# Kernel optimization log

Hardware: AMD Instinct MI355X
Metric: run time of the kernel (lower is better)

Reference implementation:

```python
import jax, jax.numpy as jnp
import numpy as np

NUM_NODES = 6144
INPUT_DIM = 128
OUTPUT_DIM = 128
NUM_HEADS = 4
HEAD_DIM = OUTPUT_DIM // NUM_HEADS
NEG_INF = -9e15  # mask constant used by the original module


def setup_inputs() -> dict:
    key = jax.random.key(0)
    k_x, k_adj, k_W, k_a = jax.random.split(key, 4)
    x = jax.random.normal(k_x, (NUM_NODES, INPUT_DIM), dtype=jnp.float32)
    adj = jax.random.randint(k_adj, (NUM_NODES, NUM_NODES), 0, 2, dtype=jnp.int32)
    # kaiming-uniform-ish init scale
    W = jax.random.uniform(k_W, (NUM_HEADS, INPUT_DIM, HEAD_DIM), dtype=jnp.float32,
                           minval=-1.0, maxval=1.0) * np.sqrt(6.0 / INPUT_DIM)
    a = jax.random.uniform(k_a, (NUM_HEADS, 2 * HEAD_DIM, 1), dtype=jnp.float32,
                           minval=-1.0, maxval=1.0) * np.sqrt(6.0 / (2 * HEAD_DIM))
    return {"x": x, "adj": adj, "W": W, "a": a}


def reference(x, adj, W, a):
    # x: [N, Din], adj: [N, N] int, W: [H, Din, d], a: [H, 2d, 1]
    H, Din, d = W.shape
    N = x.shape[0]
    h = jnp.einsum('ni,hid->hnd', x, W)               # [H, N, d] per-head projections
    a_dst = a[:, :d, 0]                                # applied to h_j (column / source of message)
    a_src = a[:, d:, 0]                                # applied to h_i (row / destination)
    s_dst = jnp.einsum('hnd,hd->hn', h, a_dst)         # [H, N]
    s_src = jnp.einsum('hnd,hd->hn', h, a_src)         # [H, N]
    # energy[h, i, j] = leaky_relu(a1 . h_j + a2 . h_i), same as concat-attention
    energy = jax.nn.leaky_relu(s_src[:, :, None] + s_dst[:, None, :], negative_slope=0.2)
    energy = jnp.where(adj[None] > 0, energy, NEG_INF)  # [H, N, N]
    attention = jax.nn.softmax(energy, axis=-1)
    h_prime = jnp.einsum('hij,hjd->hid', attention, h)  # [H, N, d]
    # faithful to torch h_prime.view(num_nodes, -1) on a contiguous [H,N,d] tensor
    return jnp.reshape(h_prime, (N, H * d))
```

## Files before the change

kernel.cpp:

```cpp
#include <hip/hip_runtime.h>
#include <stdint.h>

#define N_NODES 6144
#define LOG2E 1.44269504088896f

typedef float f32x4 __attribute__((ext_vector_type(4)));
typedef float f32x2 __attribute__((ext_vector_type(2)));
typedef short short8 __attribute__((ext_vector_type(8)));
typedef unsigned int uint32;
typedef unsigned long long uint64;

extern "C" __device__ float __ocml_native_exp2_f32(float);

__device__ __forceinline__ uint32 bitmask32(uint32 bits, int j) {
#if __has_builtin(__builtin_amdgcn_sbfe)
  return (uint32)__builtin_amdgcn_sbfe((int)bits, (uint32)j, 1u);
#else
  return (uint32)(((int)(bits << (31 - j))) >> 31);
#endif
}

__global__ __launch_bounds__(256) void k1_feat(const float* __restrict__ x,
                                               const float* __restrict__ W,
                                               const float* __restrict__ a,
                                               unsigned short* __restrict__ hfF,
                                               float* __restrict__ s_src2,
                                               float* __restrict__ s_dst2) {
  __shared__ float xA[8][132];
  __shared__ unsigned short tbp[128][12];
  int t = threadIdx.x;
  int bx = blockIdx.x;
  int n0 = bx << 3;
  {
    int row = t >> 5, c4 = (t & 31) << 2;
    *(float4*)&xA[row][c4] = *(const float4*)(x + (size_t)(n0 + row) * 128 + c4);
  }
  __syncthreads();
  int r = t & 7, cgA = t >> 3;
  int hh = cgA >> 3, d0 = (cgA & 7) << 2;
  const float* wp = W + hh * 4096 + d0;
  float ac0 = 0.f, ac1 = 0.f, ac2 = 0.f, ac3 = 0.f;
  #pragma unroll 8
  for (int i = 0; i < 128; ++i) {
    float xv = xA[r][i];
    float4 wv = *(const float4*)(wp + (i << 5));
    ac0 += xv * wv.x; ac1 += xv * wv.y;
    ac2 += xv * wv.z; ac3 += xv * wv.w;
  }
  int c0 = cgA << 2;
  tbp[c0 + 0][r] = (unsigned short)((__float_as_uint(ac0) + 0x8000u) >> 16);
  tbp[c0 + 1][r] = (unsigned short)((__float_as_uint(ac1) + 0x8000u) >> 16);
  tbp[c0 + 2][r] = (unsigned short)((__float_as_uint(ac2) + 0x8000u) >> 16);
  tbp[c0 + 3][r] = (unsigned short)((__float_as_uint(ac3) + 0x8000u) >> 16);
  float4 adv = *(const float4*)(a + hh * 64 + d0);
  float4 asv = *(const float4*)(a + hh * 64 + 32 + d0);
  float pd = ac0 * adv.x + ac1 * adv.y + ac2 * adv.z + ac3 * adv.w;
  float ps = ac0 * asv.x + ac1 * asv.y + ac2 * asv.z + ac3 * asv.w;
  pd += __shfl_xor(pd, 8); pd += __shfl_xor(pd, 16); pd += __shfl_xor(pd, 32);
  ps += __shfl_xor(ps, 8); ps += __shfl_xor(ps, 16); ps += __shfl_xor(ps, 32);
  if (((t & 63) >> 3) == 0) {
    s_dst2[hh * N_NODES + n0 + r] = pd * LOG2E;
    s_src2[hh * N_NODES + n0 + r] = ps * LOG2E;
  }
  __syncthreads();
  if (t < 128) {
    int h2 = t >> 5, ff = (t >> 4) & 1, mm = t & 15;
    const uint32* s32 = (const uint32*)&tbp[t][0];
    int4 v;
    v.x = s32[0]; v.y = s32[1]; v.z = s32[2]; v.w = s32[3];
    int kb = bx >> 2, qq = bx & 3;
    *(int4*)(hfF + (size_t)(((h2 * 192 + kb) * 2 + ff) * 64 + qq * 16 + mm) * 8) = v;
  }
}

__device__ __forceinline__ void gat_tile(float ss, uint32 bits8,
                                         const f32x2 (&dv)[4], short8 b0, short8 b1,
                                         short8 ones, f32x4& a0, f32x4& a1, f32x4& az) {
  union { uint32 u4[4]; short8 v; } afr;
  f32x2 ss2;
  ss2[0] = ss; ss2[1] = ss;
  #pragma unroll
  for (int p = 0; p < 4; ++p) {
    f32x2 e = ss2 + dv[p];
    f32x2 e5 = e * 0.2f;
    float lrl = fmaxf(e[0], e5[0]);
    float lrh = fmaxf(e[1], e5[1]);
    float exl = __ocml_native_exp2_f32(lrl);
    float exh = __ocml_native_exp2_f32(lrh);
    uint32 wl = __float_as_uint(exl) & bitmask32(bits8, 2 * p);
    uint32 wh = __float_as_uint(exh) & bitmask32(bits8, 2 * p + 1);
    uint32 pk;
    asm("v_cvt_pk_bf16_f32 %0, %1, %2"
        : "=v"(pk)
        : "v"(__uint_as_float(wl)), "v"(__uint_as_float(wh)));
    afr.u4[p] = pk;
  }
  a0 = __builtin_amdgcn_mfma_f32_16x16x32_bf16(afr.v, b0, a0, 0, 0, 0);
  a1 = __builtin_amdgcn_mfma_f32_16x16x32_bf16(afr.v, b1, a1, 0, 0, 0);
  az = __builtin_amdgcn_mfma_f32_16x16x32_bf16(afr.v, ones, az, 0, 0, 0);
}

__device__ __forceinline__ void step2(uint32 w0, uint32 w1,
                                      int sh, const float* sdp, int koff,
                                      int4 B0i, int4 B1i, short8 ones,
                                      float ss0, float ss1,
                                      f32x4& a00, f32x4& a01, f32x4& a10, f32x4& a11,
                                      f32x4& az0, f32x4& az1) {
  union { f32x4 q[2]; f32x2 d[4]; } du;
  du.q[0] = *(const f32x4*)(sdp + koff);
  du.q[1] = *(const f32x4*)(sdp + koff + 4);
  union { int4 i; short8 v; } b0u, b1u;
  b0u.i = B0i; b1u.i = B1i;
  gat_tile(ss0, (w0 >> sh), du.d, b0u.v, b1u.v, ones, a00, a01, az0);
  gat_tile(ss1, (w1 >> sh), du.d, b0u.v, b1u.v, ones, a10, a11, az1);
}

__global__ __launch_bounds__(256, 3) void k2_attn(const int* __restrict__ adj,
                                                  const unsigned short* __restrict__ hfF,
                                                  const float* __restrict__ s_src2,
                                                  const float* __restrict__ s_dst2,
                                                  float* __restrict__ Zpart,
                                                  float* __restrict__ part) {
  __shared__ float sd[4][1536];
  __shared__ uint32 mlds[2][32][4];
  int t = threadIdx.x;
  int h = t >> 6, lane = t & 63, m = lane & 15, quad = lane >> 4;
  int sh = quad << 3;
  int bx = blockIdx.x;
  int slice = bx & 3, mg = bx >> 2;
  int i0 = mg << 5, kbase = slice * 1536;

  const int* arow = adj + (size_t)(i0 + (h << 3)) * N_NODES + kbase + lane;
  int av[16];
  #pragma unroll
  for (int r = 0; r < 16; ++r)
    av[r] = arow[(r >> 1) * N_NODES + ((r & 1) << 6)];

  {
    const float4* g = (const float4*)s_dst2;
    float4* l = (float4*)sd;
    int kb4 = slice * 384;
    #pragma unroll
    for (int r = 0; r < 6; ++r) {
      int u = t + (r << 8);
      int hx = u / 384, uu = u - hx * 384;
      l[hx * 384 + uu] = g[hx * 1536 + kb4 + uu];
    }
  }
  float ss0 = s_src2[h * N_NODES + i0 + m];
  float ss1 = s_src2[h * N_NODES + i0 + 16 + m];
  #pragma unroll
  for (int r = 0; r < 16; ++r) {
    uint64 b = __ballot(av[r] != 0);
    if (lane == r)
      *(uint64*)&mlds[0][(h << 3) + (r >> 1)][(r & 1) << 1] = b;
  }
  __syncthreads();

  const unsigned short* hfb = hfF + (size_t)(h * 192 + slice * 48) * 1024 + lane * 8;
  const float* sdp = &sd[h][0] + sh;

  f32x4 a00 = {0,0,0,0}, a01 = {0,0,0,0};
  f32x4 a10 = {0,0,0,0}, a11 = {0,0,0,0};
  f32x4 az0 = {0,0,0,0}, az1 = {0,0,0,0};
  union { uint32 u[4]; short8 v; } ones;
  #pragma unroll
  for (int q = 0; q < 4; ++q) ones.u[q] = 0x3F803F80u;

  #pragma unroll 1
  for (int o = 0; o < 12; ++o) {
    int cur = o & 1, nxt = cur ^ 1;
    const unsigned short* gb = hfb + o * 4096;
    int4 B00 = *(const int4*)(gb);
    int4 B01 = *(const int4*)(gb + 512);
    int4 B10 = *(const int4*)(gb + 1024);
    int4 B11 = *(const int4*)(gb + 1536);
    int4 B20 = *(const int4*)(gb + 2048);
    int4 B21 = *(const int4*)(gb + 2560);
    int4 B30 = *(const int4*)(gb + 3072);
    int4 B31 = *(const int4*)(gb + 3584);
    int pv[16];
    if (o < 11) {
      const int* ap = arow + ((o + 1) << 7);
      #pragma unroll
      for (int r = 0; r < 16; ++r)
        pv[r] = ap[(r >> 1) * N_NODES + ((r & 1) << 6)];
    }
    uint4 M0 = *(const uint4*)&mlds[cur][m][0];
    uint4 M1 = *(const uint4*)&mlds[cur][16 + m][0];
    __builtin_amdgcn_sched_barrier(0);
    int ko = o << 7;
    step2(M0.x, M1.x, sh, sdp, ko,      B00, B01, ones.v, ss0, ss1,
          a00, a01, a10, a11, az0, az1);
    step2(M0.y, M1.y, sh, sdp, ko + 32, B10, B11, ones.v, ss0, ss1,
          a00, a01, a10, a11, az0, az1);
    step2(M0.z, M1.z, sh, sdp, ko + 64, B20, B21, ones.v, ss0, ss1,
          a00, a01, a10, a11, az0, az1);
    step2(M0.w, M1.w, sh, sdp, ko + 96, B30, B31, ones.v, ss0, ss1,
          a00, a01, a10, a11, az0, az1);
    __builtin_amdgcn_sched_barrier(0);
    if (o < 11) {
      #pragma unroll
      for (int r = 0; r < 16; ++r) {
        uint64 b = __ballot(pv[r] != 0);
        if (lane == r)
          *(uint64*)&mlds[nxt][(h << 3) + (r >> 1)][(r & 1) << 1] = b;
      }
    }
    __syncthreads();
  }

  if (m == 0) {
    float* zb = Zpart + (size_t)slice * 24576 + h * N_NODES + i0 + (quad << 2);
    #pragma unroll
    for (int r = 0; r < 4; ++r) {
      zb[r] = az0[r];
      zb[16 + r] = az1[r];
    }
  }
  float* pb = part + (size_t)slice * 786432 + (size_t)h * (N_NODES * 32) +
              (size_t)i0 * 32;
  #pragma unroll
  for (int r = 0; r < 4; ++r) {
    int row = (quad << 2) + r;
    pb[row * 32 + m] = a00[r];
    pb[row * 32 + 16 + m] = a01[r];
    pb[(16 + row) * 32 + m] = a10[r];
    pb[(16 + row) * 32 + 16 + m] = a11[r];
  }
}

__global__ __launch_bounds__(256) void k3_final(const float* __restrict__ part,
                                                const float* __restrict__ Zpart,
                                                float* __restrict__ out) {
  unsigned int idx4 = blockIdx.x * 256 + threadIdx.x;
  unsigned int h = idx4 / 49152u;
  unsigned int i = (idx4 - h * 49152u) >> 3;
  float z = 0.f;
  #pragma unroll
  for (int s = 0; s < 4; ++s) z += Zpart[s * 24576u + h * N_NODES + i];
  f32x4 p = {0.f, 0.f, 0.f, 0.f};
  const f32x4* P = (const f32x4*)part;
  #pragma unroll
  for (int s = 0; s < 4; ++s) p += P[(size_t)s * 196608u + idx4];
  float rz = 1.0f / z;
  ((f32x4*)out)[idx4] = p * rz;
}

extern "C" void kernel_launch(void* const* d_in, const int* in_sizes, int n_in,
                              void* d_out, int out_size, void* d_ws, size_t ws_size,
                              hipStream_t stream) {
  const float* x = (const float*)d_in[0];
  const int* adj = (const int*)d_in[1];
  const float* W = (const float*)d_in[2];
  const float* a = (const float*)d_in[3];
  float* out = (float*)d_out;

  float* wsf = (float*)d_ws;
  unsigned short* hfF = (unsigned short*)wsf;
  float* s_src2 = wsf + 393216;
  float* s_dst2 = s_src2 + 24576;
  float* part   = s_dst2 + 24576;
  float* Zpart  = part + 4 * 786432;

  hipLaunchKernelGGL(k1_feat, dim3(768), dim3(256), 0, stream, x, W, a, hfF, s_src2, s_dst2);
  hipLaunchKernelGGL(k2_attn, dim3(768), dim3(256), 0, stream,
                     adj, hfF, s_src2, s_dst2, Zpart, part);
  hipLaunchKernelGGL(k3_final, dim3(768), dim3(256), 0, stream, part, Zpart, out);
}
```

Baseline: 247.7 us.

## Fuse split-K reduction into attention kernel via last-block atomic counter

Removes the separate k3_final launch. Each attention block now writes its partial sums with cache-bypassing stores and bumps a per-row-group atomic counter. The fourth (last) slice block then reduces the four partials, normalises by the summed Z, and writes the output. This saves a kernel launch and a pass over the partial buffers, at the cost of fences, an atomic, and a serial tail in the last block of each group.

```diff
diff --git a/kernel.cpp b/kernel.cpp
--- a/kernel.cpp
+++ b/kernel.cpp
@@ -20,16 +20,32 @@
 #endif
 }
 
+__device__ __forceinline__ void stg_sc(float* p, float v) {
+  asm volatile("global_store_dword %0, %1, off sc0 sc1" :: "v"(p), "v"(v) : "memory");
+}
+__device__ __forceinline__ float ldg_sc(const float* p) {
+  float v;
+  asm volatile("global_load_dword %0, %1, off sc0 sc1" : "=v"(v) : "v"(p) : "memory");
+  return v;
+}
+__device__ __forceinline__ f32x4 ldg_sc4(const float* p) {
+  f32x4 v;
+  asm volatile("global_load_dwordx4 %0, %1, off sc0 sc1" : "=v"(v) : "v"(p) : "memory");
+  return v;
+}
+
 __global__ __launch_bounds__(256) void k1_feat(const float* __restrict__ x,
                                                const float* __restrict__ W,
                                                const float* __restrict__ a,
                                                unsigned short* __restrict__ hfF,
                                                float* __restrict__ s_src2,
-                                               float* __restrict__ s_dst2) {
+                                               float* __restrict__ s_dst2,
+                                               int* __restrict__ cnt) {
   __shared__ float xA[8][132];
   __shared__ unsigned short tbp[128][12];
   int t = threadIdx.x;
   int bx = blockIdx.x;
+  if (bx == 0 && t < 192) cnt[t] = 0;
   int n0 = bx << 3;
   {
     int row = t >> 5, c4 = (t & 31) << 2;
@@ -120,7 +136,9 @@
                                                   const float* __restrict__ s_src2,
                                                   const float* __restrict__ s_dst2,
                                                   float* __restrict__ Zpart,
-                                                  float* __restrict__ part) {
+                                                  float* __restrict__ part,
+                                                  int* __restrict__ cnt,
+                                                  float* __restrict__ out) {
   __shared__ float sd[4][1536];
   __shared__ uint32 mlds[2][32][4];
   int t = threadIdx.x;
@@ -214,8 +232,8 @@
     float* zb = Zpart + (size_t)slice * 24576 + h * N_NODES + i0 + (quad << 2);
     #pragma unroll
     for (int r = 0; r < 4; ++r) {
-      zb[r] = az0[r];
-      zb[16 + r] = az1[r];
+      stg_sc(zb + r, az0[r]);
+      stg_sc(zb + 16 + r, az1[r]);
     }
   }
   float* pb = part + (size_t)slice * 786432 + (size_t)h * (N_NODES * 32) +
@@ -223,28 +241,49 @@
   #pragma unroll
   for (int r = 0; r < 4; ++r) {
     int row = (quad << 2) + r;
-    pb[row * 32 + m] = a00[r];
-    pb[row * 32 + 16 + m] = a01[r];
-    pb[(16 + row) * 32 + m] = a10[r];
-    pb[(16 + row) * 32 + 16 + m] = a11[r];
-  }
-}
-
-__global__ __launch_bounds__(256) void k3_final(const float* __restrict__ part,
-                                                const float* __restrict__ Zpart,
-                                                float* __restrict__ out) {
-  unsigned int idx4 = blockIdx.x * 256 + threadIdx.x;
-  unsigned int h = idx4 / 49152u;
-  unsigned int i = (idx4 - h * 49152u) >> 3;
-  float z = 0.f;
-  #pragma unroll
-  for (int s = 0; s < 4; ++s) z += Zpart[s * 24576u + h * N_NODES + i];
-  f32x4 p = {0.f, 0.f, 0.f, 0.f};
-  const f32x4* P = (const f32x4*)part;
-  #pragma unroll
-  for (int s = 0; s < 4; ++s) p += P[(size_t)s * 196608u + idx4];
-  float rz = 1.0f / z;
-  ((f32x4*)out)[idx4] = p * rz;
+    stg_sc(pb + row * 32 + m, a00[r]);
+    stg_sc(pb + row * 32 + 16 + m, a01[r]);
+    stg_sc(pb + (16 + row) * 32 + m, a10[r]);
+    stg_sc(pb + (16 + row) * 32 + 16 + m, a11[r]);
+  }
+  __threadfence();
+  __syncthreads();
+  __shared__ int go;
+  if (t == 0) {
+    int old = __hip_atomic_fetch_add(&cnt[mg], 1, __ATOMIC_ACQ_REL,
+                                     __HIP_MEMORY_SCOPE_AGENT);
+    go = (old == 3);
+  }
+  __syncthreads();
+  if (!go) return;
+  __builtin_amdgcn_fence(__ATOMIC_ACQUIRE, "agent");
+
+  {
+    int hh = t >> 6, idx = t & 63;
+    int nl = idx >> 1, chalf = (idx & 1) << 4;
+    const float* pbase = part + (size_t)hh * (N_NODES * 32) +
+                         (size_t)(i0 + nl) * 32 + chalf;
+    f32x4 v[4][4];
+    #pragma unroll
+    for (int s = 0; s < 4; ++s)
+      #pragma unroll
+      for (int u = 0; u < 4; ++u)
+        v[s][u] = ldg_sc4(pbase + (size_t)s * 786432 + (u << 2));
+    float zv[4];
+    #pragma unroll
+    for (int s = 0; s < 4; ++s)
+      zv[s] = ldg_sc(Zpart + s * 24576 + hh * N_NODES + i0 + nl);
+    asm volatile("s_waitcnt vmcnt(0)" ::: "memory");
+    __builtin_amdgcn_sched_barrier(0);
+    float z = zv[0] + zv[1] + zv[2] + zv[3];
+    float rz = 1.0f / z;
+    float* ob = out + (size_t)hh * (N_NODES * 32) + (size_t)(i0 + nl) * 32 + chalf;
+    #pragma unroll
+    for (int u = 0; u < 4; ++u) {
+      f32x4 p = v[0][u] + v[1][u] + v[2][u] + v[3][u];
+      *(f32x4*)(ob + (u << 2)) = p * rz;
+    }
+  }
 }
 
 extern "C" void kernel_launch(void* const* d_in, const int* in_sizes, int n_in,
@@ -262,9 +301,10 @@
   float* s_dst2 = s_src2 + 24576;
   float* part   = s_dst2 + 24576;
   float* Zpart  = part + 4 * 786432;
-
-  hipLaunchKernelGGL(k1_feat, dim3(768), dim3(256), 0, stream, x, W, a, hfF, s_src2, s_dst2);
+  int* cnt      = (int*)(Zpart + 4 * 24576);
+
+  hipLaunchKernelGGL(k1_feat, dim3(768), dim3(256), 0, stream, x, W, a, hfF,
+                     s_src2, s_dst2, cnt);
   hipLaunchKernelGGL(k2_attn, dim3(768), dim3(256), 0, stream,
-                     adj, hfF, s_src2, s_dst2, Zpart, part);
-  hipLaunchKernelGGL(k3_final, dim3(768), dim3(256), 0, stream, part, Zpart, out);
-}
+                     adj, hfF, s_src2, s_dst2, Zpart, part, cnt, out);
+}
```

Result: slower. 386.5 us (+56.0%).

## Halve rows per attention block to double grid and raise occupancy

Applied to the files above, without the earlier changes.

Each k2_attn block now handles 16 destination rows instead of 32, so the grid doubles to 1536 blocks and launch bounds ask for 6 waves per SIMD instead of 3. Per-thread accumulators, adjacency prefetch registers and mask LDS are halved, which should let more blocks stay resident and hide memory latency. In exchange, every feature tile (hfF) and s_dst slice is loaded and staged into LDS twice as often per output row, so feature traffic and per-block setup grow.

```diff
diff --git a/kernel.cpp b/kernel.cpp
--- a/kernel.cpp
+++ b/kernel.cpp
@@ -100,40 +100,37 @@
   az = __builtin_amdgcn_mfma_f32_16x16x32_bf16(afr.v, ones, az, 0, 0, 0);
 }
 
-__device__ __forceinline__ void step2(uint32 w0, uint32 w1,
-                                      int sh, const float* sdp, int koff,
-                                      int4 B0i, int4 B1i, short8 ones,
-                                      float ss0, float ss1,
-                                      f32x4& a00, f32x4& a01, f32x4& a10, f32x4& a11,
-                                      f32x4& az0, f32x4& az1) {
+__device__ __forceinline__ void step1(uint32 w0, int sh, const float* sdp,
+                                      int koff, int4 B0i, int4 B1i, short8 ones,
+                                      float ss0,
+                                      f32x4& a00, f32x4& a01, f32x4& az0) {
   union { f32x4 q[2]; f32x2 d[4]; } du;
   du.q[0] = *(const f32x4*)(sdp + koff);
   du.q[1] = *(const f32x4*)(sdp + koff + 4);
   union { int4 i; short8 v; } b0u, b1u;
   b0u.i = B0i; b1u.i = B1i;
   gat_tile(ss0, (w0 >> sh), du.d, b0u.v, b1u.v, ones, a00, a01, az0);
-  gat_tile(ss1, (w1 >> sh), du.d, b0u.v, b1u.v, ones, a10, a11, az1);
-}
-
-__global__ __launch_bounds__(256, 3) void k2_attn(const int* __restrict__ adj,
+}
+
+__global__ __launch_bounds__(256, 6) void k2_attn(const int* __restrict__ adj,
                                                   const unsigned short* __restrict__ hfF,
                                                   const float* __restrict__ s_src2,
                                                   const float* __restrict__ s_dst2,
                                                   float* __restrict__ Zpart,
                                                   float* __restrict__ part) {
   __shared__ float sd[4][1536];
-  __shared__ uint32 mlds[2][32][4];
+  __shared__ uint32 mlds[2][16][4];
   int t = threadIdx.x;
   int h = t >> 6, lane = t & 63, m = lane & 15, quad = lane >> 4;
   int sh = quad << 3;
   int bx = blockIdx.x;
   int slice = bx & 3, mg = bx >> 2;
-  int i0 = mg << 5, kbase = slice * 1536;
-
-  const int* arow = adj + (size_t)(i0 + (h << 3)) * N_NODES + kbase + lane;
-  int av[16];
-  #pragma unroll
-  for (int r = 0; r < 16; ++r)
+  int i0 = mg << 4, kbase = slice * 1536;
+
+  const int* arow = adj + (size_t)(i0 + (h << 2)) * N_NODES + kbase + lane;
+  int av[8];
+  #pragma unroll
+  for (int r = 0; r < 8; ++r)
     av[r] = arow[(r >> 1) * N_NODES + ((r & 1) << 6)];
 
   {
@@ -148,21 +145,18 @@
     }
   }
   float ss0 = s_src2[h * N_NODES + i0 + m];
-  float ss1 = s_src2[h * N_NODES + i0 + 16 + m];
-  #pragma unroll
-  for (int r = 0; r < 16; ++r) {
+  #pragma unroll
+  for (int r = 0; r < 8; ++r) {
     uint64 b = __ballot(av[r] != 0);
     if (lane == r)
-      *(uint64*)&mlds[0][(h << 3) + (r >> 1)][(r & 1) << 1] = b;
+      *(uint64*)&mlds[0][(h << 2) + (r >> 1)][(r & 1) << 1] = b;
   }
   __syncthreads();
 
   const unsigned short* hfb = hfF + (size_t)(h * 192 + slice * 48) * 1024 + lane * 8;
   const float* sdp = &sd[h][0] + sh;
 
-  f32x4 a00 = {0,0,0,0}, a01 = {0,0,0,0};
-  f32x4 a10 = {0,0,0,0}, a11 = {0,0,0,0};
-  f32x4 az0 = {0,0,0,0}, az1 = {0,0,0,0};
+  f32x4 a00 = {0,0,0,0}, a01 = {0,0,0,0}, az0 = {0,0,0,0};
   union { uint32 u[4]; short8 v; } ones;
   #pragma unroll
   for (int q = 0; q < 4; ++q) ones.u[q] = 0x3F803F80u;
@@ -179,32 +173,27 @@
     int4 B21 = *(const int4*)(gb + 2560);
     int4 B30 = *(const int4*)(gb + 3072);
     int4 B31 = *(const int4*)(gb + 3584);
-    int pv[16];
+    int pv[8];
     if (o < 11) {
       const int* ap = arow + ((o + 1) << 7);
       #pragma unroll
-      for (int r = 0; r < 16; ++r)
+      for (int r = 0; r < 8; ++r)
         pv[r] = ap[(r >> 1) * N_NODES + ((r & 1) << 6)];
     }
     uint4 M0 = *(const uint4*)&mlds[cur][m][0];
-    uint4 M1 = *(const uint4*)&mlds[cur][16 + m][0];
     __builtin_amdgcn_sched_barrier(0);
     int ko = o << 7;
-    step2(M0.x, M1.x, sh, sdp, ko,      B00, B01, ones.v, ss0, ss1,
-          a00, a01, a10, a11, az0, az1);
-    step2(M0.y, M1.y, sh, sdp, ko + 32, B10, B11, ones.v, ss0, ss1,
-          a00, a01, a10, a11, az0, az1);
-    step2(M0.z, M1.z, sh, sdp, ko + 64, B20, B21, ones.v, ss0, ss1,
-          a00, a01, a10, a11, az0, az1);
-    step2(M0.w, M1.w, sh, sdp, ko + 96, B30, B31, ones.v, ss0, ss1,
-          a00, a01, a10, a11, az0, az1);
+    step1(M0.x, sh, sdp, ko,      B00, B01, ones.v, ss0, a00, a01, az0);
+    step1(M0.y, sh, sdp, ko + 32, B10, B11, ones.v, ss0, a00, a01, az0);
+    step1(M0.z, sh, sdp, ko + 64, B20, B21, ones.v, ss0, a00, a01, az0);
+    step1(M0.w, sh, sdp, ko + 96, B30, B31, ones.v, ss0, a00, a01, az0);
     __builtin_amdgcn_sched_barrier(0);
     if (o < 11) {
       #pragma unroll
-      for (int r = 0; r < 16; ++r) {
+      for (int r = 0; r < 8; ++r) {
         uint64 b = __ballot(pv[r] != 0);
         if (lane == r)
-          *(uint64*)&mlds[nxt][(h << 3) + (r >> 1)][(r & 1) << 1] = b;
+          *(uint64*)&mlds[nxt][(h << 2) + (r >> 1)][(r & 1) << 1] = b;
       }
     }
     __syncthreads();
@@ -213,10 +202,7 @@
   if (m == 0) {
     float* zb = Zpart + (size_t)slice * 24576 + h * N_NODES + i0 + (quad << 2);
     #pragma unroll
-    for (int r = 0; r < 4; ++r) {
-      zb[r] = az0[r];
-      zb[16 + r] = az1[r];
-    }
+    for (int r = 0; r < 4; ++r) zb[r] = az0[r];
   }
   float* pb = part + (size_t)slice * 786432 + (size_t)h * (N_NODES * 32) +
               (size_t)i0 * 32;
@@ -225,8 +211,6 @@
     int row = (quad << 2) + r;
     pb[row * 32 + m] = a00[r];
     pb[row * 32 + 16 + m] = a01[r];
-    pb[(16 + row) * 32 + m] = a10[r];
-    pb[(16 + row) * 32 + 16 + m] = a11[r];
   }
 }
 
@@ -263,8 +247,9 @@
   float* part   = s_dst2 + 24576;
   float* Zpart  = part + 4 * 786432;
 
-  hipLaunchKernelGGL(k1_feat, dim3(768), dim3(256), 0, stream, x, W, a, hfF, s_src2, s_dst2);
-  hipLaunchKernelGGL(k2_attn, dim3(768), dim3(256), 0, stream,
+  hipLaunchKernelGGL(k1_feat, dim3(768), dim3(256), 0, stream, x, W, a, hfF,
+                     s_src2, s_dst2);
+  hipLaunchKernelGGL(k2_attn, dim3(1536), dim3(256), 0, stream,
                      adj, hfF, s_src2, s_dst2, Zpart, part);
   hipLaunchKernelGGL(k3_final, dim3(768), dim3(256), 0, stream, part, Zpart, out);
 }
```

New measurement: 255.7 us. 3.2% more time.
